# Kernel optimization log

Measured on AMD Instinct MI355X. Metric: run time of the kernel, lower is better.

Reference implementation:

```python
import jax, jax.numpy as jnp
import numpy as np

B, C_IN, H, W = 8, 64, 64, 64
C_MID = 32


def setup_inputs() -> dict:
    key = jax.random.key(0)
    ks = jax.random.split(key, 7)
    s = 1.0 / np.sqrt(C_IN)
    return {
        "x": jax.random.normal(ks[0], (B, C_IN, H, W), dtype=jnp.float32),
        "Wk": jax.random.normal(ks[1], (C_MID, C_IN), dtype=jnp.float32) * s,
        "bk": jax.random.normal(ks[2], (C_MID,), dtype=jnp.float32) * 0.01,
        "Wq": jax.random.normal(ks[3], (C_MID, C_IN), dtype=jnp.float32) * s,
        "bq": jax.random.normal(ks[4], (C_MID,), dtype=jnp.float32) * 0.01,
        "Wv": jax.random.normal(ks[5], (C_MID, C_IN), dtype=jnp.float32) * s,
        "bv": jax.random.normal(ks[6], (C_MID,), dtype=jnp.float32) * 0.01,
    }


def reference(x, Wk, bk, Wq, bq, Wv, bv):
    # 1x1 convs == per-pixel channel projections
    def proj(Wt, bt):
        return jnp.einsum('bchw,oc->bohw', x, Wt) + bt[None, :, None, None]

    k = proj(Wk, bk)  # [B, Cm, H, W]
    q = proj(Wq, bq)
    v = proj(Wv, bv)

    b, c, h, w = q.shape
    n = h * w
    qf = q.reshape(b, c, n)
    kf = k.reshape(b, c, n)
    vf = v.reshape(b, c, n)

    # correlated_weight over spatial dims [2,3]: QK channel correlation per
    # pixel pair, softmax over key positions, weighted sum of V.
    scores = jnp.einsum('bcn,bcm->bnm', qf, kf)      # [B, N, N]
    attn = jax.nn.softmax(scores, axis=-1)
    out = jnp.einsum('bnm,bcm->bcn', attn, vf)       # [B, Cm, N]
    return out.reshape(b, c, h, w)
```

## Files before the change

### kernel.cpp

```cpp
#include <hip/hip_runtime.h>
#include <hip/hip_bf16.h>
#include <cstdint>
#include <cstddef>


typedef _Float16 f16x8 __attribute__((ext_vector_type(8)));
typedef float  f32x16 __attribute__((ext_vector_type(16)));
typedef float  f32x4  __attribute__((ext_vector_type(4)));

struct alignas(16) U4 { uint32_t w[4]; };
struct alignas(8)  U2 { uint32_t w[2]; };

#define MFMA16(A, B, C) __builtin_amdgcn_mfma_f32_32x32x16_f16((A), (B), (C), 0, 0, 0)

__device__ __forceinline__ uint16_t f2h(float f) {
    _Float16 h = (_Float16)f;
    return __builtin_bit_cast(uint16_t, h);
}
__device__ __forceinline__ uint32_t cvtpk16(float lo, float hi) {
    auto h2 = __builtin_amdgcn_cvt_pkrtz(lo, hi);
    return __builtin_bit_cast(uint32_t, h2);
}
__device__ __forceinline__ void swp(uint32_t& a, uint32_t& b) {
    asm("v_permlane32_swap_b32 %0, %1" : "+v"(a), "+v"(b));
}
__device__ __forceinline__ float ex2(float x) {
    float r;
    asm("v_exp_f32 %0, %1" : "=v"(r) : "v"(x));
    return r;
}
__device__ __forceinline__ float max3(float a, float b, float c) {
    return fmaxf(fmaxf(a, b), c);
}
__device__ __forceinline__ f16x8 ld8(const void* p) {
    return __builtin_bit_cast(f16x8, *(const U4*)p);
}

__global__ __launch_bounds__(256) void proj_kernel(
    const float* __restrict__ x,
    const float* __restrict__ Wk, const float* __restrict__ bk,
    const float* __restrict__ Wq, const float* __restrict__ bq,
    const float* __restrict__ Wv, const float* __restrict__ bv,
    uint16_t* __restrict__ qf, uint16_t* __restrict__ kf,
    uint16_t* __restrict__ vt)
{
    const int g     = blockIdx.x * 256 + threadIdx.x;
    const int pixel = g & 32767;
    const int qt    = __builtin_amdgcn_readfirstlane(g >> 15);
    const int b     = pixel >> 12;
    const int n     = pixel & 4095;
    const int ob    = qt << 2;

    const float* xb = x + (size_t)b * 64 * 4096 + n;
    float xv[64];
    #pragma unroll
    for (int ci = 0; ci < 64; ++ci) xv[ci] = xb[(size_t)ci * 4096];

    #pragma unroll
    for (int pass = 0; pass < 3; ++pass) {
        const float* W    = pass == 0 ? Wk : (pass == 1 ? Wq : Wv);
        const float* bias = pass == 0 ? bk : (pass == 1 ? bq : bv);
        float acc[4];
        #pragma unroll
        for (int o = 0; o < 4; ++o) acc[o] = bias[ob + o];
        #pragma unroll
        for (int o = 0; o < 4; ++o) {
            const float* wr = W + (size_t)(ob + o) * 64;
            #pragma unroll
            for (int ci = 0; ci < 64; ++ci)
                acc[o] = fmaf(wr[ci], xv[ci], acc[o]);
        }
        if (pass == 2) {
            #pragma unroll
            for (int o = 0; o < 4; ++o)
                vt[((size_t)(b * 32 + ob + o)) * 4096 + n] = f2h(acc[o]);
        } else {
            if (pass == 1) {
                #pragma unroll
                for (int o = 0; o < 4; ++o) acc[o] *= 1.44269504f;
            }
            U2 hp;
            #pragma unroll
            for (int j = 0; j < 2; ++j)
                hp.w[j] = (uint32_t)f2h(acc[2 * j]) | ((uint32_t)f2h(acc[2 * j + 1]) << 16);
            uint16_t* hd = (pass ? qf : kf) + ((size_t)(b * 4096 + n)) * 32 + ob;
            *(U2*)hd = hp;
        }
    }
}

__global__ __launch_bounds__(256, 4) void attn_kernel(
    const uint16_t* __restrict__ qf, const uint16_t* __restrict__ kf,
    const uint16_t* __restrict__ vt, float* __restrict__ out,
    float* __restrict__ opart, float* __restrict__ mpart,
    float* __restrict__ lpart, int ns)
{
    __shared__ __align__(16) uint16_t lk[64 * 40];
    __shared__ __align__(16) uint16_t lv[32 * 72];

    const int blk    = blockIdx.x;
    const int b      = blk & 7;
    const int rest   = blk >> 3;
    const int qblk   = rest & 31;
    const int ksp    = rest >> 5;
    const int ntiles = 64 / ns;
    const int kb0    = ksp * ntiles;
    const int kb1    = kb0 + ntiles;

    const int tid  = threadIdx.x;
    const int wv   = tid >> 6;
    const int lane = tid & 63;
    const int l31  = lane & 31;
    const int h32  = lane >> 5;
    const int qrow = qblk * 128 + wv * 32 + l31;

    f16x8 q0, q1;
    {
        const uint16_t* r = qf + ((size_t)(b * 4096 + qrow)) * 32;
        q0 = ld8(r + h32 * 8);
        q1 = ld8(r + 16 + h32 * 8);
    }

    f32x16 oacc;
    #pragma unroll
    for (int i = 0; i < 16; ++i) oacc[i] = 0.f;
    float m_run = -3.0e38f, l_run = 0.f;

    const U4* gk = (const U4*)(kf + ((size_t)b * 4096) * 32);
    const uint16_t* gv = vt + ((size_t)b * 32) * 4096;

    #pragma unroll 1
    for (int kb = kb0; kb < kb1; ++kb) {
        {
            U4 a = gk[kb * 256 + tid];
            U4 v = *(const U4*)(gv + ((size_t)(tid >> 3)) * 4096 + kb * 64 + (tid & 7) * 8);
            *(U4*)((char*)lk + (tid >> 2) * 80 + (tid & 3) * 16) = a;
            *(U4*)((char*)lv + (tid >> 3) * 144 + (tid & 7) * 16) = v;
        }
        __syncthreads();

        f32x16 s0, s1;
        #pragma unroll
        for (int i = 0; i < 16; ++i) { s0[i] = 0.f; s1[i] = 0.f; }
        {
            const char* kr = (const char*)lk + l31 * 80 + h32 * 16;
            f16x8 a0 = ld8(kr);
            f16x8 a1 = ld8(kr + 32);
            const char* kr2 = (const char*)lk + (32 + l31) * 80 + h32 * 16;
            f16x8 c0 = ld8(kr2);
            f16x8 c1 = ld8(kr2 + 32);
            s0 = MFMA16(a0, q0, s0);
            s1 = MFMA16(c0, q0, s1);
            s0 = MFMA16(a1, q1, s0);
            s1 = MFMA16(c1, q1, s1);
        }

        float mx[4];
        #pragma unroll
        for (int i = 0; i < 4; ++i)
            mx[i] = max3(max3(s0[i], s0[i + 4], s0[i + 8]),
                         max3(s0[i + 12], s1[i], s1[i + 4]),
                         fmaxf(s1[i + 8], s1[i + 12]));
        float pm = fmaxf(max3(mx[0], mx[1], mx[2]), mx[3]);
        pm = fmaxf(pm, __shfl_xor(pm, 32));

        if (__any(pm > m_run)) {
            float mn  = fmaxf(m_run, pm);
            float scl = ex2(m_run - mn);
            l_run *= scl;
            #pragma unroll
            for (int i = 0; i < 16; ++i) oacc[i] *= scl;
            m_run = mn;
        }

        #pragma unroll
        for (int i = 0; i < 16; ++i) {
            s0[i] = ex2(s0[i] - m_run);
            s1[i] = ex2(s1[i] - m_run);
        }
        float sm[8];
        #pragma unroll
        for (int i = 0; i < 8; ++i)
            sm[i] = (s0[i] + s0[i + 8]) + (s1[i] + s1[i + 8]);
        #pragma unroll
        for (int i = 0; i < 4; ++i) sm[i] += sm[i + 4];
        float rs = (sm[0] + sm[2]) + (sm[1] + sm[3]);
        rs += __shfl_xor(rs, 32);
        l_run += rs;

        U4 f1, f2, f3, f4;
        {
            uint32_t A = cvtpk16(s0[0], s0[1]),  B = cvtpk16(s0[4], s0[5]);   swp(A, B);
            uint32_t C = cvtpk16(s0[2], s0[3]),  D = cvtpk16(s0[6], s0[7]);   swp(C, D);
            f1.w[0] = A; f1.w[1] = C; f1.w[2] = B; f1.w[3] = D;
            A = cvtpk16(s0[8], s0[9]);   B = cvtpk16(s0[12], s0[13]);  swp(A, B);
            C = cvtpk16(s0[10], s0[11]); D = cvtpk16(s0[14], s0[15]);  swp(C, D);
            f2.w[0] = A; f2.w[1] = C; f2.w[2] = B; f2.w[3] = D;
            A = cvtpk16(s1[0], s1[1]);   B = cvtpk16(s1[4], s1[5]);    swp(A, B);
            C = cvtpk16(s1[2], s1[3]);   D = cvtpk16(s1[6], s1[7]);    swp(C, D);
            f3.w[0] = A; f3.w[1] = C; f3.w[2] = B; f3.w[3] = D;
            A = cvtpk16(s1[8], s1[9]);   B = cvtpk16(s1[12], s1[13]);  swp(A, B);
            C = cvtpk16(s1[10], s1[11]); D = cvtpk16(s1[14], s1[15]);  swp(C, D);
            f4.w[0] = A; f4.w[1] = C; f4.w[2] = B; f4.w[3] = D;
        }

        {
            const char* vr = (const char*)lv + l31 * 144 + h32 * 16;
            f16x8 v0 = ld8(vr);
            f16x8 v1 = ld8(vr + 32);
            f16x8 v2 = ld8(vr + 64);
            f16x8 v3 = ld8(vr + 96);
            oacc = MFMA16(v0, __builtin_bit_cast(f16x8, f1), oacc);
            oacc = MFMA16(v1, __builtin_bit_cast(f16x8, f2), oacc);
            oacc = MFMA16(v2, __builtin_bit_cast(f16x8, f3), oacc);
            oacc = MFMA16(v3, __builtin_bit_cast(f16x8, f4), oacc);
        }
        __syncthreads();
    }

    if (ns == 1) {
        const float inv = 1.f / l_run;
        float* ob = out + ((size_t)b * 32) * 4096 + qrow;
        #pragma unroll
        for (int i = 0; i < 16; ++i) {
            int c = (i & 3) + 8 * (i >> 2) + 4 * h32;
            ob[(size_t)c * 4096] = oacc[i] * inv;
        }
    } else {
        float* op = opart + ((size_t)((ksp * 8 + b) * 32)) * 4096 + qrow;
        #pragma unroll
        for (int i = 0; i < 16; ++i) {
            int c = (i & 3) + 8 * (i >> 2) + 4 * h32;
            op[(size_t)c * 4096] = oacc[i];
        }
        if (h32 == 0) {
            mpart[((size_t)(ksp * 8 + b)) * 4096 + qrow] = m_run;
            lpart[((size_t)(ksp * 8 + b)) * 4096 + qrow] = l_run;
        }
    }
}

__global__ __launch_bounds__(256) void reduce_kernel(
    const float* __restrict__ opart, const float* __restrict__ mpart,
    const float* __restrict__ lpart, float* __restrict__ out, int ns)
{
    const int idx = blockIdx.x * 256 + threadIdx.x;
    const int nq  = idx & 1023;
    const int c   = (idx >> 10) & 31;
    const int b   = idx >> 15;
    const size_t noff = (size_t)nq * 4;

    f32x4 M;
    #pragma unroll
    for (int e = 0; e < 4; ++e) M[e] = -3.0e38f;
    for (int s = 0; s < ns; ++s) {
        f32x4 mm = *(const f32x4*)(mpart + ((size_t)(s * 8 + b)) * 4096 + noff);
        #pragma unroll
        for (int e = 0; e < 4; ++e) M[e] = fmaxf(M[e], mm[e]);
    }
    f32x4 L, O;
    #pragma unroll
    for (int e = 0; e < 4; ++e) { L[e] = 0.f; O[e] = 0.f; }
    for (int s = 0; s < ns; ++s) {
        f32x4 mm = *(const f32x4*)(mpart + ((size_t)(s * 8 + b)) * 4096 + noff);
        f32x4 ll = *(const f32x4*)(lpart + ((size_t)(s * 8 + b)) * 4096 + noff);
        f32x4 oo = *(const f32x4*)(opart + ((size_t)((s * 8 + b) * 32 + c)) * 4096 + noff);
        #pragma unroll
        for (int e = 0; e < 4; ++e) {
            float w = ex2(mm[e] - M[e]);
            L[e] += ll[e] * w;
            O[e] += oo[e] * w;
        }
    }
    f32x4 r;
    #pragma unroll
    for (int e = 0; e < 4; ++e) r[e] = O[e] / L[e];
    *(f32x4*)(out + ((size_t)(b * 32 + c)) * 4096 + noff) = r;
}

extern "C" void kernel_launch(void* const* d_in, const int* in_sizes, int n_in,
                              void* d_out, int out_size, void* d_ws, size_t ws_size,
                              hipStream_t stream)
{
    (void)in_sizes; (void)n_in; (void)out_size;
    const float* x  = (const float*)d_in[0];
    const float* Wk = (const float*)d_in[1];
    const float* bk = (const float*)d_in[2];
    const float* Wq = (const float*)d_in[3];
    const float* bq = (const float*)d_in[4];
    const float* Wv = (const float*)d_in[5];
    const float* bv = (const float*)d_in[6];
    float* out = (float*)d_out;

    char* ws = (char*)d_ws;
    const size_t SZ = (size_t)8 * 4096 * 32 * 2;
    uint16_t* qf = (uint16_t*)(ws);
    uint16_t* kf = (uint16_t*)(ws + SZ);
    uint16_t* vt = (uint16_t*)(ws + 2 * SZ);
    const size_t base = 3 * SZ;

    const size_t OB  = (size_t)8 * 32 * 4096 * 4;
    const size_t MB_ = (size_t)8 * 4096 * 4;
    int ns = 1;
    if      (ws_size >= base + 8 * (OB + 2 * MB_)) ns = 8;
    else if (ws_size >= base + 4 * (OB + 2 * MB_)) ns = 4;
    else if (ws_size >= base + 2 * (OB + 2 * MB_)) ns = 2;

    float* opart = (float*)(ws + base);
    float* mpart = (float*)(ws + base + (size_t)ns * OB);
    float* lpart = (float*)(ws + base + (size_t)ns * OB + (size_t)ns * MB_);

    proj_kernel<<<1024, 256, 0, stream>>>(x, Wk, bk, Wq, bq, Wv, bv,
                                          qf, kf, vt);
    attn_kernel<<<ns * 256, 256, 0, stream>>>(qf, kf, vt, out,
                                              opart, mpart, lpart, ns);
    if (ns > 1)
        reduce_kernel<<<1024, 256, 0, stream>>>(opart, mpart, lpart, out, ns);
}
```

Baseline: 65.54 us.

## Double-buffer K/V tiles via direct global-to-LDS loads with XOR swizzled layouts

The attention loop now stages K and V tiles with global_load_lds straight into two LDS buffers, prefetching the next tile while computing the current one. This removes the register round-trip and one barrier per iteration. The projection kernel writes K and V in an XOR-swizzled order so the unpadded LDS reads avoid bank conflicts. The key split is capped at 4 instead of 8, which lowers reduction traffic but leaves fewer attention blocks in flight.

```diff
diff --git a/kernel.cpp b/kernel.cpp
--- a/kernel.cpp
+++ b/kernel.cpp
@@ -34,6 +34,11 @@
 }
 __device__ __forceinline__ f16x8 ld8(const void* p) {
     return __builtin_bit_cast(f16x8, *(const U4*)p);
+}
+__device__ __forceinline__ void gload16(const void* g, void* l) {
+    __builtin_amdgcn_global_load_lds(
+        (const __attribute__((address_space(1))) void*)g,
+        (__attribute__((address_space(3))) void*)l, 16, 0, 0);
 }
 
 __global__ __launch_bounds__(256) void proj_kernel(
@@ -72,8 +77,11 @@
         }
         if (pass == 2) {
             #pragma unroll
-            for (int o = 0; o < 4; ++o)
-                vt[((size_t)(b * 32 + ob + o)) * 4096 + n] = f2h(acc[o]);
+            for (int o = 0; o < 4; ++o) {
+                int c   = ob + o;
+                int nsw = (n & ~0x38) | ((((n >> 3) & 7) ^ (c & 7)) << 3);
+                vt[((size_t)(b * 32 + c)) * 4096 + nsw] = f2h(acc[o]);
+            }
         } else {
             if (pass == 1) {
                 #pragma unroll
@@ -83,8 +91,13 @@
             #pragma unroll
             for (int j = 0; j < 2; ++j)
                 hp.w[j] = (uint32_t)f2h(acc[2 * j]) | ((uint32_t)f2h(acc[2 * j + 1]) << 16);
-            uint16_t* hd = (pass ? qf : kf) + ((size_t)(b * 4096 + n)) * 32 + ob;
-            *(U2*)hd = hp;
+            if (pass == 0) {
+                char* rowb = (char*)kf + ((size_t)(b * 4096 + n)) * 64;
+                *(U2*)(rowb + (((qt >> 1) ^ (n & 3)) * 16) + (qt & 1) * 8) = hp;
+            } else {
+                uint16_t* hd = qf + ((size_t)(b * 4096 + n)) * 32 + ob;
+                *(U2*)hd = hp;
+            }
         }
     }
 }
@@ -95,8 +108,8 @@
     float* __restrict__ opart, float* __restrict__ mpart,
     float* __restrict__ lpart, int ns)
 {
-    __shared__ __align__(16) uint16_t lk[64 * 40];
-    __shared__ __align__(16) uint16_t lv[32 * 72];
+    __shared__ __align__(16) char lds_k[2][4096];
+    __shared__ __align__(16) char lds_v[2][4096];
 
     const int blk    = blockIdx.x;
     const int b      = blk & 7;
@@ -108,7 +121,7 @@
     const int kb1    = kb0 + ntiles;
 
     const int tid  = threadIdx.x;
-    const int wv   = tid >> 6;
+    const int wv   = __builtin_amdgcn_readfirstlane(tid >> 6);
     const int lane = tid & 63;
     const int l31  = lane & 31;
     const int h32  = lane >> 5;
@@ -126,29 +139,43 @@
     for (int i = 0; i < 16; ++i) oacc[i] = 0.f;
     float m_run = -3.0e38f, l_run = 0.f;
 
-    const U4* gk = (const U4*)(kf + ((size_t)b * 4096) * 32);
-    const uint16_t* gv = vt + ((size_t)b * 32) * 4096;
-
-    #pragma unroll 1
+    const char* gk = (const char*)kf + ((size_t)b * 4096) * 64;
+    const char* gv = (const char*)vt
+                   + ((size_t)(b * 32 + wv * 8 + (lane >> 3))) * 8192
+                   + (lane & 7) * 16;
+    const char* gk_l = gk + wv * 1024 + lane * 16;
+
+    const int ka0 = l31 * 64 + ((h32 ^ (l31 & 3)) * 16);
+    const int ka1 = l31 * 64 + (((2 + h32) ^ (l31 & 3)) * 16);
+    int vo[4];
+    #pragma unroll
+    for (int j = 0; j < 4; ++j)
+        vo[j] = l31 * 128 + (((h32 + 2 * j) ^ (l31 & 7)) * 16);
+
+    {
+        gload16(gk_l + (size_t)kb0 * 4096, lds_k[kb0 & 1] + wv * 1024);
+        gload16(gv   + (size_t)kb0 * 128,  lds_v[kb0 & 1] + wv * 1024);
+    }
+
+    #pragma unroll 2
     for (int kb = kb0; kb < kb1; ++kb) {
-        {
-            U4 a = gk[kb * 256 + tid];
-            U4 v = *(const U4*)(gv + ((size_t)(tid >> 3)) * 4096 + kb * 64 + (tid & 7) * 8);
-            *(U4*)((char*)lk + (tid >> 2) * 80 + (tid & 3) * 16) = a;
-            *(U4*)((char*)lv + (tid >> 3) * 144 + (tid & 7) * 16) = v;
-        }
+        const int cur = kb & 1;
         __syncthreads();
+
+        if (kb + 1 < kb1) {
+            gload16(gk_l + (size_t)(kb + 1) * 4096, lds_k[cur ^ 1] + wv * 1024);
+            gload16(gv   + (size_t)(kb + 1) * 128,  lds_v[cur ^ 1] + wv * 1024);
+        }
 
         f32x16 s0, s1;
         #pragma unroll
         for (int i = 0; i < 16; ++i) { s0[i] = 0.f; s1[i] = 0.f; }
         {
-            const char* kr = (const char*)lk + l31 * 80 + h32 * 16;
-            f16x8 a0 = ld8(kr);
-            f16x8 a1 = ld8(kr + 32);
-            const char* kr2 = (const char*)lk + (32 + l31) * 80 + h32 * 16;
-            f16x8 c0 = ld8(kr2);
-            f16x8 c1 = ld8(kr2 + 32);
+            const char* lk = lds_k[cur];
+            f16x8 a0 = ld8(lk + ka0);
+            f16x8 a1 = ld8(lk + ka1);
+            f16x8 c0 = ld8(lk + 2048 + ka0);
+            f16x8 c1 = ld8(lk + 2048 + ka1);
             s0 = MFMA16(a0, q0, s0);
             s1 = MFMA16(c0, q0, s1);
             s0 = MFMA16(a1, q1, s0);
@@ -205,17 +232,16 @@
         }
 
         {
-            const char* vr = (const char*)lv + l31 * 144 + h32 * 16;
-            f16x8 v0 = ld8(vr);
-            f16x8 v1 = ld8(vr + 32);
-            f16x8 v2 = ld8(vr + 64);
-            f16x8 v3 = ld8(vr + 96);
+            const char* lv = lds_v[cur];
+            f16x8 v0 = ld8(lv + vo[0]);
+            f16x8 v1 = ld8(lv + vo[1]);
+            f16x8 v2 = ld8(lv + vo[2]);
+            f16x8 v3 = ld8(lv + vo[3]);
             oacc = MFMA16(v0, __builtin_bit_cast(f16x8, f1), oacc);
             oacc = MFMA16(v1, __builtin_bit_cast(f16x8, f2), oacc);
             oacc = MFMA16(v2, __builtin_bit_cast(f16x8, f3), oacc);
             oacc = MFMA16(v3, __builtin_bit_cast(f16x8, f4), oacc);
         }
-        __syncthreads();
     }
 
     if (ns == 1) {
@@ -302,8 +328,7 @@
     const size_t OB  = (size_t)8 * 32 * 4096 * 4;
     const size_t MB_ = (size_t)8 * 4096 * 4;
     int ns = 1;
-    if      (ws_size >= base + 8 * (OB + 2 * MB_)) ns = 8;
-    else if (ws_size >= base + 4 * (OB + 2 * MB_)) ns = 4;
+    if      (ws_size >= base + 4 * (OB + 2 * MB_)) ns = 4;
     else if (ws_size >= base + 2 * (OB + 2 * MB_)) ns = 2;
 
     float* opart = (float*)(ws + base);
```

New measurement: 63.86 us. 1.03x faster.
